# Kernel tuning notes

Measured on AMD Instinct MI355X. Metric: run time of the kernel, lower is better.

The kernel has to match this reference:

```python
import jax, jax.numpy as jnp
import numpy as np

VOCAB = 23      # prime -> all nonzero scales invertible mod VOCAB
LEN = 256
BATCH = 512
HIDDEN = 4096
TEMP = 0.1


def _inv_table(v):
    # multiplicative inverse table mod v; inv(0) := 0 (non-invertible element)
    return np.array([0] + [pow(a, -1, v) for a in range(1, v)], dtype=np.int32)


def st_one_hot_argmax(x, temperature):
    """Straight-through one-hot argmax with tempered-softmax gradient."""
    soft = jax.nn.softmax(x / temperature, axis=-1)
    hard = jax.nn.one_hot(jnp.argmax(x, axis=-1), x.shape[-1], dtype=x.dtype)
    return soft + jax.lax.stop_gradient(hard - soft)


def one_hot_minus(inputs, shift):
    """(inputs - shift) % V in one-hot space via circular convolution."""
    V = inputs.shape[-1]
    # shift_matrix[..., u, v] = shift[..., (v - u) % V]  (== roll(shift, u))
    idx = (jnp.arange(V)[None, :] - jnp.arange(V)[:, None]) % V  # [u, v]
    shift_matrix = shift[..., idx]                               # [..., u, v]
    return jnp.einsum('...v,...uv->...u', inputs, shift_matrix)


def one_hot_multiply(inputs, scale):
    """(inputs * scale) % V in one-hot space; scale=0 component is dropped."""
    V = inputs.shape[-1]
    perm = (jnp.arange(V)[:, None] * jnp.arange(V)[None, :]) % V  # [a, v]
    P = jax.nn.one_hot(perm, V, dtype=inputs.dtype)               # [a, v, u]
    scale0 = scale * (jnp.arange(V) != 0).astype(scale.dtype)     # zero a=0 row
    return jnp.einsum('...v,...a,avu->...u', inputs, scale0, P)


def multiplicative_inverse(scale, v):
    """One-hot multiplicative inverse mod v via constant lookup table."""
    Inv = jax.nn.one_hot(jnp.asarray(_inv_table(v)), v, dtype=scale.dtype)  # [a, u]
    return jnp.einsum('...a,au->...u', scale, Inv)


def setup_inputs() -> dict:
    key = jax.random.key(0)
    k1, k2, k3 = jax.random.split(key, 3)
    tokens = jax.random.randint(k1, (BATCH, LEN), 0, VOCAB)
    inputs = jax.nn.one_hot(tokens, VOCAB, dtype=jnp.float32)     # [B, L, V]
    mask = (jnp.arange(LEN) % 2).astype(jnp.float32)[:, None]     # [L, 1]
    s1 = 1.0 / np.sqrt(LEN * VOCAB)
    s2 = 1.0 / np.sqrt(HIDDEN)
    W1 = jax.random.normal(k2, (LEN * VOCAB, HIDDEN), dtype=jnp.float32) * s1
    b1 = jnp.zeros((HIDDEN,), dtype=jnp.float32)
    W2 = jax.random.normal(k3, (HIDDEN, LEN * 2 * VOCAB), dtype=jnp.float32) * s2
    b2 = jnp.zeros((LEN * 2 * VOCAB,), dtype=jnp.float32)
    return {"inputs": inputs, "mask": mask, "W1": W1, "b1": b1, "W2": W2, "b2": b2}


def reference(inputs, mask, W1, b1, W2, b2):
    B, L, V = inputs.shape
    masked_inputs = mask * inputs                                 # [B, L, V]
    # layer(mask * inputs): flatten -> MLP -> [B, L, 2V]
    h = jax.nn.relu(masked_inputs.reshape(B, L * V) @ W1 + b1)
    net = (h @ W2 + b2).reshape(B, L, 2 * V)
    loc, scale = net[..., :V], net[..., V:]
    loc = st_one_hot_argmax(loc, TEMP)
    scale = st_one_hot_argmax(scale, TEMP)
    inv_scale = multiplicative_inverse(scale, V)
    shifted = one_hot_minus(inputs, loc)
    masked_outputs = (1.0 - mask) * one_hot_multiply(shifted, inv_scale)
    return masked_inputs + masked_outputs
```

## Files before the change

kernel.cpp:

```cpp
#include <hip/hip_runtime.h>
#include <cstddef>
#include <cstdint>

#define VOC 23
#define SEQ 256
#define NB  512
#define HID 4096
#define NCOL 11776
#define NPK 5888
#define KP  12288
#define EPS_TIE 4e-5f

__constant__ int INV23[VOC] = {0,1,12,8,6,14,4,10,3,18,7,21,2,16,5,20,13,19,9,17,15,11,22};

typedef __attribute__((ext_vector_type(8))) short short8;
typedef __attribute__((ext_vector_type(4))) float f32x4;

static __device__ __forceinline__ unsigned int f2bf(float f) {
  unsigned int x = __float_as_uint(f);
  return (x + 0x7fffu + ((x >> 16) & 1u)) >> 16;
}
static __device__ __forceinline__ float bf2f(unsigned int u) {
  return __uint_as_float(u << 16);
}

#define GL2LDS(g, l) __builtin_amdgcn_global_load_lds(                      \
    (const __attribute__((address_space(1))) unsigned int*)(g),             \
    (__attribute__((address_space(3))) unsigned int*)(l), 16, 0, 0)

__global__ __launch_bounds__(256) void k_tok_copy(const float* __restrict__ in,
                                                  float* __restrict__ out,
                                                  int* __restrict__ tok) {
  const int b = blockIdx.x;
  const int l = threadIdx.x;
  const float* row = in + ((size_t)b * SEQ + l) * VOC;
  int t = 0; float best = -1.0f;
#pragma unroll
  for (int v = 0; v < VOC; ++v) { float x = row[v]; if (x > best) { best = x; t = v; } }
  tok[b * SEQ + l] = t;
  if (l & 1) {
    float* o = out + ((size_t)b * SEQ + l) * VOC;
#pragma unroll
    for (int v = 0; v < VOC; ++v) o[v] = row[v];
  }
}

__global__ __launch_bounds__(256) void k_pack_w2(const float* __restrict__ W2,
                                                 unsigned short* __restrict__ Bp) {
  const int k0 = blockIdx.x * 64;
  const int j0 = blockIdx.y * 64;
  const int tid = threadIdx.x;
  __shared__ float T[64 * 65];
#pragma unroll
  for (int it = 0; it < 16; ++it) {
    int idx = it * 256 + tid;
    int k_l = idx >> 6, j_l = idx & 63;
    int j = j0 + j_l;
    int ee = j / 46, cc = j - ee * 46;
    T[j_l * 65 + k_l] = W2[(size_t)(k0 + k_l) * NCOL + 92 * ee + cc];
  }
  __syncthreads();
  const int j_l = tid >> 2, qt = tid & 3;
  unsigned int d[24];
#pragma unroll
  for (int pr = 0; pr < 8; ++pr) {
    int k_l = qt * 16 + pr * 2;
    float va = T[j_l * 65 + k_l], vb = T[j_l * 65 + k_l + 1];
    unsigned int ha = f2bf(va), la = f2bf(va - bf2f(ha));
    unsigned int hb = f2bf(vb), lb = f2bf(vb - bf2f(hb));
    d[pr * 3 + 0] = ha | (la << 16);
    d[pr * 3 + 1] = ha | (hb << 16);
    d[pr * 3 + 2] = lb | (hb << 16);
  }
  char* dst = ((char*)Bp) + (size_t)(j0 + j_l) * (KP * 2) + 6 * k0 + 96 * qt;
#pragma unroll
  for (int u = 0; u < 6; ++u) {
    uint4 w = make_uint4(d[4 * u], d[4 * u + 1], d[4 * u + 2], d[4 * u + 3]);
    ((uint4*)dst)[u] = w;
  }
}

__global__ __launch_bounds__(256) void k_hidden(const float* __restrict__ W1,
                                                const float* __restrict__ b1,
                                                const int* __restrict__ tok,
                                                float* __restrict__ h,
                                                unsigned short* __restrict__ Ap) {
  const int b = blockIdx.x;
  const int tid = threadIdx.x;
  __shared__ int rowS[128];
  if (tid < 128) {
    const int l = 2 * tid + 1;
    rowS[tid] = l * VOC + tok[b * SEQ + l];
  }
  __syncthreads();
  float4 acc[4];
#pragma unroll
  for (int j = 0; j < 4; ++j) acc[j] = make_float4(0.f, 0.f, 0.f, 0.f);
  for (int i = 0; i < 128; i += 2) {
    const float4* wr0 = (const float4*)(W1 + (size_t)rowS[i] * HID);
    const float4* wr1 = (const float4*)(W1 + (size_t)rowS[i + 1] * HID);
    float4 w0[4], w1[4];
#pragma unroll
    for (int j = 0; j < 4; ++j) w0[j] = wr0[tid + 256 * j];
#pragma unroll
    for (int j = 0; j < 4; ++j) w1[j] = wr1[tid + 256 * j];
#pragma unroll
    for (int j = 0; j < 4; ++j) {
      acc[j].x += w0[j].x; acc[j].y += w0[j].y; acc[j].z += w0[j].z; acc[j].w += w0[j].w;
      acc[j].x += w1[j].x; acc[j].y += w1[j].y; acc[j].z += w1[j].z; acc[j].w += w1[j].w;
    }
  }
  float4* hb = (float4*)(h + (size_t)b * HID);
  const float4* bv = (const float4*)b1;
#pragma unroll
  for (int j = 0; j < 4; ++j) {
    float4 bb = bv[tid + 256 * j];
    float4 r;
    r.x = fmaxf(acc[j].x + bb.x, 0.f);
    r.y = fmaxf(acc[j].y + bb.y, 0.f);
    r.z = fmaxf(acc[j].z + bb.z, 0.f);
    r.w = fmaxf(acc[j].w + bb.w, 0.f);
    hb[tid + 256 * j] = r;
    unsigned int h0 = f2bf(r.x), L0 = f2bf(r.x - bf2f(h0));
    unsigned int h1 = f2bf(r.y), L1 = f2bf(r.y - bf2f(h1));
    unsigned int h2 = f2bf(r.z), L2 = f2bf(r.z - bf2f(h2));
    unsigned int h3 = f2bf(r.w), L3 = f2bf(r.w - bf2f(h3));
    uint2* ap = (uint2*)(((char*)Ap) + (size_t)b * (KP * 2) + 24 * (tid + 256 * j));
    ap[0] = make_uint2(h0 | (h0 << 16), L0 | (h1 << 16));
    ap[1] = make_uint2(h1 | (L1 << 16), h2 | (h2 << 16));
    ap[2] = make_uint2(L2 | (h3 << 16), h3 | (L3 << 16));
  }
}

__global__ __launch_bounds__(512, 2) void k3_mfma(const unsigned short* __restrict__ Ap,
                                                  const unsigned short* __restrict__ Bp,
                                                  float* __restrict__ partial) {
  __shared__ char lds3[4 * 32768];
  const int tid = threadIdx.x;

  const int f = blockIdx.x;
  const int d = (f & 7) * 23 + (f >> 3);
  const int g = d >> 1, mi = d & 1;
  const int s = g / 23, n = g - s * 23;
  const int bm0 = mi * 256;
  const int bn0 = n * 256;
  const int kb0 = s * 6144;

  const int lane = tid & 63, wave = tid >> 6;
  const int wm = wave & 1, wn = wave >> 1;
  const int r = lane & 15, q = lane >> 4;

  size_t gsrc[4]; int gdst[4];
#pragma unroll
  for (int c = 0; c < 4; ++c) {
    const int G = (c & 1) * 512 + tid;
    const int line = G >> 3, gph = G & 7;
    const int gin = gph ^ (line & 7);
    const int grow = 2 * line + (gin >> 2);
    const int gcol = (gin & 3) << 4;
    const int row0 = (c < 2 ? bm0 : bn0) + grow;
    gsrc[c] = (size_t)row0 * (KP * 2) + gcol;
    gdst[c] = G * 16;
  }

#define STAGE3(slot, kbv) do {                                                    \
    char* ldsb_ = lds3 + ((slot) << 15);                                          \
    GL2LDS(((const char*)Ap) + gsrc[0] + (kbv), ldsb_ + gdst[0]);                 \
    GL2LDS(((const char*)Ap) + gsrc[1] + (kbv), ldsb_ + gdst[1]);                 \
    GL2LDS(((const char*)Bp) + gsrc[2] + (kbv), ldsb_ + 16384 + gdst[2]);         \
    GL2LDS(((const char*)Bp) + gsrc[3] + (kbv), ldsb_ + 16384 + gdst[3]);         \
  } while (0)

  const int gphR = (((((r & 1) << 2) | q) ^ ((r >> 1) & 7)) << 4);
  const int aoff = (wm * 64 + (r >> 1)) * 128 + gphR;
  const int boff = (wn * 32 + (r >> 1)) * 128 + gphR;

  f32x4 acc[8][4];
#pragma unroll
  for (int i = 0; i < 8; ++i)
#pragma unroll
    for (int j = 0; j < 4; ++j) acc[i][j] = (f32x4){0.f, 0.f, 0.f, 0.f};

#define COMPUTE3(slot) do {                                                       \
    const char* sb_ = lds3 + ((slot) << 15);                                      \
    short8 a_[8], b_[4];                                                          \
    _Pragma("unroll")                                                             \
    for (int i_ = 0; i_ < 8; ++i_)                                                \
      a_[i_] = *(const short8*)(sb_ + aoff + i_ * 1024);                          \
    _Pragma("unroll")                                                             \
    for (int j_ = 0; j_ < 4; ++j_)                                                \
      b_[j_] = *(const short8*)(sb_ + 16384 + boff + j_ * 1024);                  \
    __builtin_amdgcn_s_setprio(1);                                                \
    _Pragma("unroll")                                                             \
    for (int i_ = 0; i_ < 8; ++i_)                                                \
      _Pragma("unroll")                                                           \
      for (int j_ = 0; j_ < 4; ++j_)                                              \
        acc[i_][j_] = __builtin_amdgcn_mfma_f32_16x16x32_bf16(a_[i_], b_[j_],     \
                                                              acc[i_][j_], 0, 0, 0); \
    __builtin_amdgcn_s_setprio(0);                                                \
  } while (0)

  STAGE3(0, kb0);
  STAGE3(1, kb0 + 64);
  STAGE3(2, kb0 + 128);

#pragma unroll 1
  for (int t = 0; t < 93; ++t) {
    asm volatile("s_waitcnt vmcnt(8)" ::: "memory");
    __builtin_amdgcn_s_barrier();
    __builtin_amdgcn_sched_barrier(0);
    const int slot = t & 3;
    {
      const char* sb_ = lds3 + (slot << 15);
      short8 a_[8], b_[4];
#pragma unroll
      for (int i_ = 0; i_ < 8; ++i_)
        a_[i_] = *(const short8*)(sb_ + aoff + i_ * 1024);
#pragma unroll
      for (int j_ = 0; j_ < 4; ++j_)
        b_[j_] = *(const short8*)(sb_ + 16384 + boff + j_ * 1024);
      STAGE3((t + 3) & 3, kb0 + (t + 3) * 64);
      __builtin_amdgcn_s_setprio(1);
#pragma unroll
      for (int i_ = 0; i_ < 8; ++i_)
#pragma unroll
        for (int j_ = 0; j_ < 4; ++j_)
          acc[i_][j_] = __builtin_amdgcn_mfma_f32_16x16x32_bf16(a_[i_], b_[j_],
                                                                acc[i_][j_], 0, 0, 0);
      __builtin_amdgcn_s_setprio(0);
    }
  }
  asm volatile("s_waitcnt vmcnt(8)" ::: "memory");
  __builtin_amdgcn_s_barrier();
  __builtin_amdgcn_sched_barrier(0);
  COMPUTE3(93 & 3);
  asm volatile("s_waitcnt vmcnt(4)" ::: "memory");
  __builtin_amdgcn_s_barrier();
  __builtin_amdgcn_sched_barrier(0);
  COMPUTE3(94 & 3);
  asm volatile("s_waitcnt vmcnt(0)" ::: "memory");
  __builtin_amdgcn_s_barrier();
  __builtin_amdgcn_sched_barrier(0);
  COMPUTE3(95 & 3);

  float* pbase = partial + (size_t)s * NB * NPK;
#pragma unroll
  for (int i = 0; i < 8; ++i) {
    const int m = bm0 + wm * 128 + 16 * i + 4 * q;
#pragma unroll
    for (int j = 0; j < 4; ++j) {
      const int nn = bn0 + wn * 64 + 16 * j + r;
      float* pp = pbase + (size_t)m * NPK + nn;
#pragma unroll
      for (int reg = 0; reg < 4; ++reg)
        pp[(size_t)reg * NPK] = acc[i][j][reg];
    }
  }
#undef STAGE3
#undef COMPUTE3
}

__global__ __launch_bounds__(256) void k_epilogue(const float* __restrict__ partial,
                                                  const float* __restrict__ b2,
                                                  const int* __restrict__ tok,
                                                  int* __restrict__ win,
                                                  int* __restrict__ gcnt,
                                                  int* __restrict__ glist,
                                                  float* __restrict__ out) {
  const int b = blockIdx.x, tid = threadIdx.x;
  const int e = tid >> 1, grp = tid & 1;
  __shared__ int winS[256];
  __shared__ int flagS[256];
  float x[VOC];
  const size_t base = (size_t)b * NPK + 46 * e + 23 * grp;
#pragma unroll
  for (int c = 0; c < VOC; ++c) x[c] = b2[92 * e + 23 * grp + c];
#pragma unroll
  for (int s2 = 0; s2 < 4; ++s2) {
    const float* pp = partial + (size_t)s2 * NB * NPK + base;
#pragma unroll
    for (int c = 0; c < VOC; ++c) x[c] += pp[c];
  }
  float b0 = -1e30f, b1v = -1e30f; int bi = 0;
#pragma unroll
  for (int c = 0; c < VOC; ++c) {
    if (x[c] > b0) { b1v = b0; b0 = x[c]; bi = c; }
    else if (x[c] > b1v) b1v = x[c];
  }
  winS[tid] = bi;
  flagS[tid] = (b0 - b1v < EPS_TIE) ? 1 : 0;
  __syncthreads();
  if (!grp) {
    const int loc = winS[tid], sc = winS[tid + 1];
    win[b * 256 + 2 * e] = loc;
    win[b * 256 + 2 * e + 1] = sc;
    const int f0 = flagS[tid], f1 = flagS[tid + 1];
    if (f0 | f1) {
      int idx = atomicAdd(gcnt, 1);
      glist[idx] = e | (b << 7) | (f0 << 16) | (f1 << 17);
    }
    const int l = 2 * e;
    float* o = out + ((size_t)b * SEQ + l) * VOC;
    if (sc == 0) {
      for (int v = 0; v < VOC; ++v) o[v] = 0.f;
    } else {
      const int t = tok[b * SEQ + l];
      int dd = t - loc; if (dd < 0) dd += VOC;
      const int u = (INV23[sc] * dd) % VOC;
      for (int v = 0; v < VOC; ++v) o[v] = (v == u) ? 1.f : 0.f;
    }
  }
}

__global__ __launch_bounds__(192) void k_recheck(const float* __restrict__ h,
                                                 const float* __restrict__ W2,
                                                 const float* __restrict__ b2,
                                                 const int* __restrict__ tok,
                                                 const int* __restrict__ win,
                                                 const int* __restrict__ gcnt,
                                                 const int* __restrict__ glist,
                                                 float* __restrict__ out) {
  const int tid = threadIdx.x;
  __shared__ double dpart[184];
  __shared__ double dlog[VOC];
  __shared__ int decS[2];
  const int n = gcnt[0];
  for (int ei = blockIdx.x; ei < n; ei += 128) {
    const int ent = glist[ei];
    const int e = ent & 127, b = (ent >> 7) & 511;
    const int l = 2 * e;
#pragma unroll
    for (int grp = 0; grp < 2; ++grp) {
      if (!(ent & (1 << (16 + grp)))) {
        if (tid == 0) decS[grp] = win[b * 256 + 2 * e + grp];
      } else {
        const int col0 = 92 * e + 23 * grp;
        if (tid < 184) {
          const int c = tid >> 3, part = tid & 7;
          const float* hb = h + (size_t)b * HID;
          const size_t colc = (size_t)(col0 + c);
          double sacc[8] = {0, 0, 0, 0, 0, 0, 0, 0};
          const int kbase = part * 512;
          for (int kk = 0; kk < 512; kk += 8) {
#pragma unroll
            for (int t2 = 0; t2 < 8; ++t2) {
              const int k = kbase + kk + t2;
              sacc[t2] += (double)hb[k] * (double)W2[(size_t)k * NCOL + colc];
            }
          }
          dpart[tid] = ((sacc[0] + sacc[1]) + (sacc[2] + sacc[3])) +
                       ((sacc[4] + sacc[5]) + (sacc[6] + sacc[7]));
        }
        __syncthreads();
        if (tid < VOC) {
          double sd = (double)b2[col0 + tid];
#pragma unroll
          for (int p2 = 0; p2 < 8; ++p2) sd += dpart[tid * 8 + p2];
          dlog[tid] = sd;
        }
        __syncthreads();
        if (tid == 0) {
          double best = -1e300; int bi2 = 0;
#pragma unroll
          for (int c = 0; c < VOC; ++c)
            if (dlog[c] > best) { best = dlog[c]; bi2 = c; }
          decS[grp] = bi2;
        }
      }
      __syncthreads();
    }
    if (tid < VOC) {
      const int loc = decS[0], sc = decS[1];
      float val = 0.f;
      if (sc != 0) {
        const int t = tok[b * SEQ + l];
        int dd = t - loc; if (dd < 0) dd += VOC;
        const int u = (INV23[sc] * dd) % VOC;
        val = (tid == u) ? 1.f : 0.f;
      }
      out[((size_t)b * SEQ + l) * VOC + tid] = val;
    }
    __syncthreads();
  }
}

extern "C" void kernel_launch(void* const* d_in, const int* in_sizes, int n_in,
                              void* d_out, int out_size, void* d_ws, size_t ws_size,
                              hipStream_t stream) {
  const float* in  = (const float*)d_in[0];
  const float* W1  = (const float*)d_in[2];
  const float* b1  = (const float*)d_in[3];
  const float* W2  = (const float*)d_in[4];
  const float* b2  = (const float*)d_in[5];
  float* out = (float*)d_out;

  char* w = (char*)d_ws;
  int* tok = (int*)w;                         w += (size_t)NB * SEQ * 4;
  float* h = (float*)w;                       w += (size_t)NB * HID * 4;
  unsigned short* Ap = (unsigned short*)w;    w += (size_t)NB * KP * 2;
  unsigned short* Bp = (unsigned short*)w;    w += (size_t)NPK * KP * 2;
  float* partial = (float*)w;                 w += (size_t)4 * NB * NPK * 4;
  int* win = (int*)w;                         w += (size_t)NB * 256 * 4;
  int* gcnt = (int*)w;                        w += 256;
  int* glist = (int*)w;                       w += (size_t)65536 * 4;

  k_tok_copy<<<dim3(NB), dim3(256), 0, stream>>>(in, out, tok);
  k_pack_w2<<<dim3(64, 92), dim3(256), 0, stream>>>(W2, Bp);
  k_hidden<<<dim3(NB), dim3(256), 0, stream>>>(W1, b1, tok, h, Ap);
  hipMemsetAsync(gcnt, 0, 4, stream);
  k3_mfma<<<dim3(184), dim3(512), 0, stream>>>(Ap, Bp, partial);
  k_epilogue<<<dim3(NB), dim3(256), 0, stream>>>(partial, b2, tok, win, gcnt, glist, out);
  k_recheck<<<dim3(128), dim3(192), 0, stream>>>(h, W2, b2, tok, win, gcnt, glist, out);
}
```

Baseline: 621.9 us.

## Retile hidden-layer gather so each block covers eight batch rows and a column slice

The embedding-style gather-sum over W1 rows changes shape. Before, each block handled one batch row across all 4096 hidden columns with float4 loads. Now each block handles eight batch rows over a 512-column slice, using scalar coalesced loads and a precomputed row-index array written by the token kernel. The aim is to improve cache reuse of W1 rows shared between batches and columns, at the cost of narrower loads, less work in flight per thread, and 2-byte scattered stores for the split-bf16 packed activations. The token kernel now writes tok only for even positions, and the memset is hoisted to the start of the launch sequence.

```diff
diff --git a/kernel.cpp b/kernel.cpp
--- a/kernel.cpp
+++ b/kernel.cpp
@@ -28,20 +28,23 @@
     (const __attribute__((address_space(1))) unsigned int*)(g),             \
     (__attribute__((address_space(3))) unsigned int*)(l), 16, 0, 0)
 
-__global__ __launch_bounds__(256) void k_tok_copy(const float* __restrict__ in,
-                                                  float* __restrict__ out,
-                                                  int* __restrict__ tok) {
+__global__ __launch_bounds__(256) void k_tok(const float* __restrict__ in,
+                                             float* __restrict__ out,
+                                             int* __restrict__ tok,
+                                             int* __restrict__ rowIdx) {
   const int b = blockIdx.x;
   const int l = threadIdx.x;
   const float* row = in + ((size_t)b * SEQ + l) * VOC;
   int t = 0; float best = -1.0f;
 #pragma unroll
   for (int v = 0; v < VOC; ++v) { float x = row[v]; if (x > best) { best = x; t = v; } }
-  tok[b * SEQ + l] = t;
   if (l & 1) {
+    rowIdx[b * 128 + (l >> 1)] = l * VOC + t;
     float* o = out + ((size_t)b * SEQ + l) * VOC;
 #pragma unroll
     for (int v = 0; v < VOC; ++v) o[v] = row[v];
+  } else {
+    tok[b * SEQ + l] = t;
   }
 }
 
@@ -80,55 +83,35 @@
   }
 }
 
-__global__ __launch_bounds__(256) void k_hidden(const float* __restrict__ W1,
-                                                const float* __restrict__ b1,
-                                                const int* __restrict__ tok,
-                                                float* __restrict__ h,
-                                                unsigned short* __restrict__ Ap) {
-  const int b = blockIdx.x;
+__global__ __launch_bounds__(256) void k_hidden2(const float* __restrict__ W1,
+                                                 const float* __restrict__ b1,
+                                                 const int* __restrict__ rowIdx,
+                                                 float* __restrict__ h,
+                                                 unsigned short* __restrict__ Ap) {
   const int tid = threadIdx.x;
-  __shared__ int rowS[128];
-  if (tid < 128) {
-    const int l = 2 * tid + 1;
-    rowS[tid] = l * VOC + tok[b * SEQ + l];
-  }
-  __syncthreads();
-  float4 acc[4];
-#pragma unroll
-  for (int j = 0; j < 4; ++j) acc[j] = make_float4(0.f, 0.f, 0.f, 0.f);
-  for (int i = 0; i < 128; i += 2) {
-    const float4* wr0 = (const float4*)(W1 + (size_t)rowS[i] * HID);
-    const float4* wr1 = (const float4*)(W1 + (size_t)rowS[i + 1] * HID);
-    float4 w0[4], w1[4];
-#pragma unroll
-    for (int j = 0; j < 4; ++j) w0[j] = wr0[tid + 256 * j];
-#pragma unroll
-    for (int j = 0; j < 4; ++j) w1[j] = wr1[tid + 256 * j];
-#pragma unroll
-    for (int j = 0; j < 4; ++j) {
-      acc[j].x += w0[j].x; acc[j].y += w0[j].y; acc[j].z += w0[j].z; acc[j].w += w0[j].w;
-      acc[j].x += w1[j].x; acc[j].y += w1[j].y; acc[j].z += w1[j].z; acc[j].w += w1[j].w;
-    }
-  }
-  float4* hb = (float4*)(h + (size_t)b * HID);
-  const float4* bv = (const float4*)b1;
-#pragma unroll
-  for (int j = 0; j < 4; ++j) {
-    float4 bb = bv[tid + 256 * j];
-    float4 r;
-    r.x = fmaxf(acc[j].x + bb.x, 0.f);
-    r.y = fmaxf(acc[j].y + bb.y, 0.f);
-    r.z = fmaxf(acc[j].z + bb.z, 0.f);
-    r.w = fmaxf(acc[j].w + bb.w, 0.f);
-    hb[tid + 256 * j] = r;
-    unsigned int h0 = f2bf(r.x), L0 = f2bf(r.x - bf2f(h0));
-    unsigned int h1 = f2bf(r.y), L1 = f2bf(r.y - bf2f(h1));
-    unsigned int h2 = f2bf(r.z), L2 = f2bf(r.z - bf2f(h2));
-    unsigned int h3 = f2bf(r.w), L3 = f2bf(r.w - bf2f(h3));
-    uint2* ap = (uint2*)(((char*)Ap) + (size_t)b * (KP * 2) + 24 * (tid + 256 * j));
-    ap[0] = make_uint2(h0 | (h0 << 16), L0 | (h1 << 16));
-    ap[1] = make_uint2(h1 | (L1 << 16), h2 | (h2 << 16));
-    ap[2] = make_uint2(L2 | (h3 << 16), h3 | (L3 << 16));
+  const int x = blockIdx.x & 7;
+  const int s = blockIdx.x >> 3;
+  const int b0 = s * 8;
+#pragma unroll 1
+  for (int p = 0; p < 2; ++p) {
+    const int col = x * 512 + p * 256 + tid;
+    const float bb = b1[col];
+#pragma unroll 1
+    for (int bi = 0; bi < 8; ++bi) {
+      const int b = b0 + bi;
+      const int* rp = rowIdx + b * 128;
+      float acc = 0.f;
+#pragma unroll 16
+      for (int i = 0; i < 128; ++i)
+        acc += W1[(size_t)rp[i] * HID + col];
+      const float r = fmaxf(acc + bb, 0.f);
+      h[(size_t)b * HID + col] = r;
+      const unsigned int hi = f2bf(r), lo = f2bf(r - bf2f(hi));
+      unsigned short* ap = (unsigned short*)(((char*)Ap) + (size_t)b * (KP * 2) + 6 * col);
+      ap[0] = (unsigned short)hi;
+      ap[1] = (unsigned short)hi;
+      ap[2] = (unsigned short)lo;
+    }
   }
 }
 
@@ -403,11 +386,12 @@
   int* win = (int*)w;                         w += (size_t)NB * 256 * 4;
   int* gcnt = (int*)w;                        w += 256;
   int* glist = (int*)w;                       w += (size_t)65536 * 4;
-
-  k_tok_copy<<<dim3(NB), dim3(256), 0, stream>>>(in, out, tok);
+  int* rowIdx = (int*)w;                      w += (size_t)NB * 128 * 4;
+
+  hipMemsetAsync(gcnt, 0, 4, stream);
+  k_tok<<<dim3(NB), dim3(256), 0, stream>>>(in, out, tok, rowIdx);
+  k_hidden2<<<dim3(512), dim3(256), 0, stream>>>(W1, b1, rowIdx, h, Ap);
   k_pack_w2<<<dim3(64, 92), dim3(256), 0, stream>>>(W2, Bp);
-  k_hidden<<<dim3(NB), dim3(256), 0, stream>>>(W1, b1, tok, h, Ap);
-  hipMemsetAsync(gcnt, 0, 4, stream);
   k3_mfma<<<dim3(184), dim3(512), 0, stream>>>(Ap, Bp, partial);
   k_epilogue<<<dim3(NB), dim3(256), 0, stream>>>(partial, b2, tok, win, gcnt, glist, out);
   k_recheck<<<dim3(128), dim3(192), 0, stream>>>(h, W2, b2, tok, win, gcnt, glist, out);
```

New measurement: 612.1 us. About the same (-1.6%).
